# Kernel optimization log

Hardware: AMD Instinct MI355X
Metric: run time of the kernel (lower is better)

Reference implementation:

```python
import jax, jax.numpy as jnp
import numpy as np
from jax import lax

NC = 8  # num_classes
NUM_ITERS = 2


def _resize_bilinear_ac(x, out_h, out_w):
    """Bilinear resize with align_corners=True, x: (N, C, H, W)."""
    N, C, H, W = x.shape

    def coords(n_out, n_in):
        if n_out == 1:
            return jnp.zeros((1,), jnp.float32)
        return jnp.linspace(0.0, float(n_in - 1), n_out, dtype=jnp.float32)

    ys = coords(out_h, H)
    xs = coords(out_w, W)
    y0 = jnp.floor(ys).astype(jnp.int32)
    y1 = jnp.minimum(y0 + 1, H - 1)
    wy = (ys - y0.astype(jnp.float32)).astype(x.dtype)
    x0 = jnp.floor(xs).astype(jnp.int32)
    x1 = jnp.minimum(x0 + 1, W - 1)
    wx = (xs - x0.astype(jnp.float32)).astype(x.dtype)

    r0 = x[:, :, y0, :]
    r1 = x[:, :, y1, :]
    r = r0 * (1.0 - wy)[None, None, :, None] + r1 * wy[None, None, :, None]
    c0 = r[:, :, :, x0]
    c1 = r[:, :, :, x1]
    return c0 * (1.0 - wx)[None, None, None, :] + c1 * wx[None, None, None, :]


def _conv2d(x, w, groups=1):
    k = w.shape[-1]
    pad = k // 2
    return lax.conv_general_dilated(
        x, w, window_strides=(1, 1), padding=[(pad, pad), (pad, pad)],
        dimension_numbers=('NCHW', 'OIHW', 'NCHW'), feature_group_count=groups)


def _mean_field_update(unary, guidance, spatial_w, bilateral_w, compat_w):
    Q = jax.nn.softmax(unary, axis=1)
    cw = compat_w[:, :, 0, 0]  # (O, I)
    for _ in range(NUM_ITERS):
        spatial_msg = _conv2d(Q, spatial_w, groups=NC)          # depthwise 3x3
        bilateral_in = jnp.concatenate([Q, guidance], axis=1)   # (N, NC+6, H, W)
        bilateral_msg = _conv2d(bilateral_in, bilateral_w)      # 3x3 dense
        message = spatial_msg + bilateral_msg
        message = jnp.einsum('nchw,oc->nohw', message, cw)      # 1x1 compat conv
        Q = jax.nn.softmax(unary - message, axis=1)
    return Q


def setup_inputs() -> dict:
    key = jax.random.key(0)
    ks = jax.random.split(key, 16)
    inp = {
        'logits': jax.random.normal(ks[0], (8, NC, 512, 512), jnp.float32),
        'image': jax.random.uniform(ks[1], (8, 3, 512, 512), jnp.float32),
        'skip0': jax.random.normal(ks[2], (8, 64, 256, 256), jnp.float32),
        'skip1': jax.random.normal(ks[3], (8, 128, 128, 128), jnp.float32),
        'skip2': jax.random.normal(ks[4], (8, 256, 64, 64), jnp.float32),
        'skip3': jax.random.normal(ks[5], (8, 512, 32, 32), jnp.float32),
        'spatial_w': jax.random.normal(ks[6], (NC, 1, 3, 3), jnp.float32) * 0.1,
        'bilateral_w': jax.random.normal(ks[7], (NC, NC + 6, 3, 3), jnp.float32) * 0.1,
        # compat_conv is initialized to -I (zeros then -= eye) in the module
        'compat_w': (-jnp.eye(NC, dtype=jnp.float32)).reshape(NC, NC, 1, 1),
        'skip_w0': jax.random.normal(ks[8], (3, 64, 1, 1), jnp.float32) * 0.05,
        'skip_b0': jnp.zeros((3,), jnp.float32),
        'skip_w1': jax.random.normal(ks[9], (3, 128, 1, 1), jnp.float32) * 0.05,
        'skip_b1': jnp.zeros((3,), jnp.float32),
        'skip_w2': jax.random.normal(ks[10], (3, 256, 1, 1), jnp.float32) * 0.05,
        'skip_b2': jnp.zeros((3,), jnp.float32),
        'skip_w3': jax.random.normal(ks[11], (3, 512, 1, 1), jnp.float32) * 0.05,
        'skip_b3': jnp.zeros((3,), jnp.float32),
    }
    return inp


def reference(logits, image, skip0, skip1, skip2, skip3,
              spatial_w, bilateral_w, compat_w,
              skip_w0, skip_b0, skip_w1, skip_b1,
              skip_w2, skip_b2, skip_w3, skip_b3):
    H, W = logits.shape[2], logits.shape[3]

    # fuse_skip_features: 1x1 project each skip to 3ch, upsample, average
    skips = [skip0, skip1, skip2, skip3]
    ws = [skip_w0, skip_w1, skip_w2, skip_w3]
    bs = [skip_b0, skip_b1, skip_b2, skip_b3]
    fused = jnp.zeros((logits.shape[0], 3, H, W), logits.dtype)
    for feat, w, b in zip(skips, ws, bs):
        p = jnp.einsum('nchw,oc->nohw', feat, w[:, :, 0, 0]) + b[None, :, None, None]
        fused = fused + _resize_bilinear_ac(p, H, W)
    fused = fused / len(skips)

    guidance = jnp.concatenate([image, fused], axis=1)  # (N, 6, H, W)

    Q_full = _mean_field_update(logits, guidance, spatial_w, bilateral_w, compat_w)

    logits_down = _resize_bilinear_ac(logits, H // 2, W // 2)
    guidance_down = _resize_bilinear_ac(guidance, H // 2, W // 2)
    Q_down = _mean_field_update(logits_down, guidance_down, spatial_w, bilateral_w, compat_w)
    Q_down_up = _resize_bilinear_ac(Q_down, H, W)

    return (Q_full + Q_down_up) / 2.0
```

## Files before the change

kernel.cpp:

```cpp
#include <hip/hip_runtime.h>
#include <hip/hip_fp16.h>
#include <math.h>

#define NB 8
#define NCLS 8
#define NGU 6
#define NBI 14
#define HF 512
#define WF 512
#define HH 256
#define WH 256

#define TOX 32
#define TOY 16
#define SX 36
#define SY 20
#define SPX (SY * SX)
#define R1W 36
#define R1N (18 * 36)
#define R1T 41
#define R2N (TOX * TOY)
#define R2T 32

typedef _Float16 f16x8 __attribute__((ext_vector_type(8)));
typedef float f32x4 __attribute__((ext_vector_type(4)));

static __device__ __forceinline__ void ac_prep(int o, float scale, int insz,
                                               int& i0, int& i1, float& f) {
    float s = (float)o * scale;
    int ii = (int)floorf(s);
    if (ii > insz - 1) ii = insz - 1;
    if (ii < 0) ii = 0;
    i0 = ii;
    i1 = (ii + 1 < insz) ? (ii + 1) : (insz - 1);
    f = s - (float)ii;
}

__global__ void k_fill_bias(float* __restrict__ out, const float* __restrict__ b, int HW) {
    int total = NB * 3 * HW;
    int idx = blockIdx.x * blockDim.x + threadIdx.x;
    if (idx >= total) return;
    int o = (idx / HW) % 3;
    out[idx] = b[o];
}

template <bool DIRECT>
__global__ void k_skip_proj(const float* __restrict__ feat, const float* __restrict__ w,
                            const float* __restrict__ b, float* __restrict__ out,
                            int C, int HW, int nch) {
    __shared__ float sw[3 * 512];
    for (int i = threadIdx.x; i < 3 * C; i += blockDim.x) sw[i] = w[i];
    __syncthreads();
    int total = NB * HW * nch;
    for (int idx = blockIdx.x * blockDim.x + threadIdx.x; idx < total;
         idx += gridDim.x * blockDim.x) {
        int hw = idx % HW;
        int t = idx / HW;
        int ch = t % nch;
        int n = t / nch;
        int c0 = ch * 64;
        const float* fp = feat + ((size_t)n * C + c0) * HW + hw;
        float a0 = 0.f, a1 = 0.f, a2 = 0.f;
        #pragma unroll 8
        for (int c = 0; c < 64; ++c) {
            float v = fp[(size_t)c * HW];
            a0 = fmaf(sw[c0 + c], v, a0);
            a1 = fmaf(sw[C + c0 + c], v, a1);
            a2 = fmaf(sw[2 * C + c0 + c], v, a2);
        }
        float* op = out + (size_t)n * 3 * HW + hw;
        if (DIRECT) {
            op[0] = b[0] + a0;
            op[HW] = b[1] + a1;
            op[2 * HW] = b[2] + a2;
        } else {
            atomicAdd(&op[0], a0);
            atomicAdd(&op[HW], a1);
            atomicAdd(&op[2 * HW], a2);
        }
    }
}

__global__ void k_fused_guid(const float* __restrict__ image,
                             const float* __restrict__ p0, const float* __restrict__ p1,
                             const float* __restrict__ p2, const float* __restrict__ p3,
                             float* __restrict__ guid) {
    const int HW = HF * WF;
    int total = NB * HW;
    int idx = blockIdx.x * blockDim.x + threadIdx.x;
    if (idx >= total) return;
    int n = idx / HW, r = idx - n * HW;
    int y = r / WF, x = r - y * WF;

    const float* ps[4] = {p0, p1, p2, p3};
    const int ss[4] = {256, 128, 64, 32};
    float f[3] = {0.f, 0.f, 0.f};
    #pragma unroll
    for (int l = 0; l < 4; ++l) {
        int s = ss[l];
        float scale = (float)(s - 1) / 511.0f;
        int y0, y1, x0, x1;
        float fy, fx;
        ac_prep(y, scale, s, y0, y1, fy);
        ac_prep(x, scale, s, x0, x1, fx);
        const float* pb = ps[l] + (size_t)n * 3 * s * s;
        #pragma unroll
        for (int o = 0; o < 3; ++o) {
            const float* pp = pb + (size_t)o * s * s;
            float v00 = pp[y0 * s + x0], v01 = pp[y0 * s + x1];
            float v10 = pp[y1 * s + x0], v11 = pp[y1 * s + x1];
            float r0 = v00 * (1.f - fy) + v10 * fy;
            float r1 = v01 * (1.f - fy) + v11 * fy;
            f[o] += r0 * (1.f - fx) + r1 * fx;
        }
    }
    float* gp = guid + (size_t)n * NGU * HW + y * WF + x;
    const float* ip = image + (size_t)n * 3 * HW + y * WF + x;
    #pragma unroll
    for (int o = 0; o < 3; ++o) gp[(size_t)o * HW] = ip[(size_t)o * HW];
    #pragma unroll
    for (int o = 0; o < 3; ++o) gp[(size_t)(3 + o) * HW] = f[o] * 0.25f;
}

__global__ void k_prep_w(const float* __restrict__ wsp, const float* __restrict__ wbil,
                         const float* __restrict__ cw, float* __restrict__ W2) {
    int i = blockIdx.x * blockDim.x + threadIdx.x;
    if (i >= NBI * 9 * 8) return;
    int o = i & 7;
    int t = (i >> 3) % 9;
    int ci = i / 72;
    float s = 0.f;
    for (int c = 0; c < NCLS; ++c)
        s += cw[o * NCLS + c] * wbil[((size_t)c * NBI + ci) * 9 + t];
    if (ci < NCLS) s += cw[o * NCLS + ci] * wsp[ci * 9 + t];
    W2[ci * 72 + t * 8 + o] = s;
}

__global__ void k_prep_frag(const float* __restrict__ W2, _Float16* __restrict__ wf) {
    int i = blockIdx.x * blockDim.x + threadIdx.x;
    if (i >= 5 * 64) return;
    int j = i >> 6, l = i & 63;
    int col = l & 15, kg = l >> 4;
    #pragma unroll
    for (int e = 0; e < 8; ++e) {
        int k = j * 32 + kg * 8 + e;
        int tap = k >> 4, ci = k & 15;
        float v = (tap < 9 && ci < 14 && col < 8) ? W2[ci * 72 + tap * 8 + col] : 0.f;
        wf[i * 8 + e] = (_Float16)v;
    }
}

template <bool DOWN, bool UPFOLD>
__global__ __launch_bounds__(256, 4) void k_mf_mfma(
    const float* __restrict__ unary, const float* __restrict__ guid,
    const float* __restrict__ Qd, float* __restrict__ Qout,
    const _Float16* __restrict__ wfragG, int H, int W, int Hs, int Ws) {
    __shared__ __align__(16) _Float16 s_t[16 + SPX * 16 + 32];
    __shared__ __align__(16) _Float16 s_msg[R1N * 8];
    _Float16* tb = s_t + 16;

    const int tid = threadIdx.x;
    const int lane = tid & 63;
    const int wv = tid >> 6;
    const int n = blockIdx.z;
    const int gx0 = blockIdx.x * TOX;
    const int gy0 = blockIdx.y * TOY;
    const int HW = H * W;
    const int HWs = Hs * Ws;
    const float* ubase = unary + (size_t)n * NCLS * HWs;
    const float* gbase = guid + (size_t)n * NGU * HWs;

    f16x8 wf[5];
    #pragma unroll
    for (int j = 0; j < 5; ++j)
        wf[j] = *(const f16x8*)(wfragG + (j * 64 + lane) * 8);

    if (tid < 16) s_t[tid] = (_Float16)0.f;
    if (tid >= 16 && tid < 48) s_t[16 + SPX * 16 + (tid - 16)] = (_Float16)0.f;

    const float syc = DOWN ? (float)(Hs - 1) / (float)(H - 1) : 1.f;
    const float sxc = DOWN ? (float)(Ws - 1) / (float)(W - 1) : 1.f;
    for (int i = tid; i < SPX; i += 256) {
        int yy = i / SX, xx = i - yy * SX;
        int gy = gy0 + yy - 2, gx = gx0 + xx - 2;
        f16x8 qv, gv;
        #pragma unroll
        for (int o = 0; o < 8; ++o) { qv[o] = (_Float16)0.f; gv[o] = (_Float16)0.f; }
        if ((unsigned)gy < (unsigned)H && (unsigned)gx < (unsigned)W) {
            float u[8], g[6];
            if (DOWN) {
                int y0, y1, x0, x1;
                float fy, fx;
                ac_prep(gy, syc, Hs, y0, y1, fy);
                ac_prep(gx, sxc, Ws, x0, x1, fx);
                const float w00 = (1.f - fy) * (1.f - fx), w01 = (1.f - fy) * fx;
                const float w10 = fy * (1.f - fx), w11 = fy * fx;
                const size_t o00 = (size_t)y0 * Ws + x0, o01 = (size_t)y0 * Ws + x1;
                const size_t o10 = (size_t)y1 * Ws + x0, o11 = (size_t)y1 * Ws + x1;
                #pragma unroll
                for (int o = 0; o < 8; ++o) {
                    const float* up = ubase + (size_t)o * HWs;
                    u[o] = w00 * up[o00] + w01 * up[o01] + w10 * up[o10] + w11 * up[o11];
                }
                #pragma unroll
                for (int c = 0; c < 6; ++c) {
                    const float* gp = gbase + (size_t)c * HWs;
                    g[c] = w00 * gp[o00] + w01 * gp[o01] + w10 * gp[o10] + w11 * gp[o11];
                }
            } else {
                const size_t off = (size_t)gy * W + gx;
                #pragma unroll
                for (int o = 0; o < 8; ++o) u[o] = ubase[(size_t)o * HWs + off];
                #pragma unroll
                for (int c = 0; c < 6; ++c) g[c] = gbase[(size_t)c * HWs + off];
            }
            float e[8];
            float s = 0.f;
            #pragma unroll
            for (int o = 0; o < 8; ++o) { e[o] = __expf(u[o]); s += e[o]; }
            float inv = 1.f / s;
            #pragma unroll
            for (int o = 0; o < 8; ++o) qv[o] = (_Float16)(e[o] * inv);
            #pragma unroll
            for (int c = 0; c < 6; ++c) gv[c] = (_Float16)g[c];
        }
        *(f16x8*)(tb + i * 16) = qv;
        *(f16x8*)(tb + i * 16 + 8) = gv;
    }
    __syncthreads();

    for (int t = wv; t < R1T; t += 4) {
        int pb = t * 16;
        int p = pb + (lane & 15);
        if (p > R1N - 1) p = R1N - 1;
        int qy = p / R1W;
        int yy = 1 + qy, xx = p - qy * R1W;
        int kg = lane >> 4;
        f32x4 acc = {0.f, 0.f, 0.f, 0.f};
        #pragma unroll
        for (int j = 0; j < 5; ++j) {
            int tap = 2 * j + (kg >> 1);
            if (tap > 8) tap = 8;
            int dy = tap / 3 - 1, dx = tap - (tap / 3) * 3 - 1;
            int idx = (yy + dy) * SX + (xx + dx);
            f16x8 af = *(const f16x8*)(tb + idx * 16 + (kg & 1) * 8);
            acc = __builtin_amdgcn_mfma_f32_16x16x32_f16(af, wf[j], acc, 0, 0, 0);
        }
        int ch = lane & 15;
        if (ch < 8) {
            int pxb = pb + (lane >> 4) * 4;
            #pragma unroll
            for (int r = 0; r < 4; ++r) {
                int px = pxb + r;
                if (px < R1N) s_msg[px * 8 + ch] = (_Float16)acc[r];
            }
        }
    }
    __syncthreads();

    for (int i = tid; i < R1N; i += 256) {
        int qy = i / R1W;
        int yy = 1 + qy, xx = i - qy * R1W;
        int gy = gy0 + yy - 2, gx = gx0 + xx - 2;
        if ((unsigned)gy < (unsigned)H && (unsigned)gx < (unsigned)W) {
            f16x8 m = *(const f16x8*)(s_msg + i * 8);
            f16x8 q0 = *(const f16x8*)(tb + (i + SX) * 16);
            float e[8];
            float s = 0.f;
            #pragma unroll
            for (int o = 0; o < 8; ++o) {
                e[o] = (float)q0[o] * __expf(-(float)m[o]);
                s += e[o];
            }
            float inv = 1.f / s;
            f16x8 q1;
            #pragma unroll
            for (int o = 0; o < 8; ++o) q1[o] = (_Float16)(e[o] * inv);
            *(f16x8*)(tb + (i + SX) * 16) = q1;
        }
    }
    f16x8 m1r[2];
    #pragma unroll
    for (int u2 = 0; u2 < 2; ++u2) {
        int i = tid + 256 * u2;
        int oy = i >> 5, ox = i & 31;
        int r1 = (1 + oy) * R1W + (2 + ox);
        m1r[u2] = *(const f16x8*)(s_msg + r1 * 8);
    }
    __syncthreads();

    for (int t = wv; t < R2T; t += 4) {
        int pb = t * 16;
        int p = pb + (lane & 15);
        int yy = 2 + (p >> 5), xx = 2 + (p & 31);
        int kg = lane >> 4;
        f32x4 acc = {0.f, 0.f, 0.f, 0.f};
        #pragma unroll
        for (int j = 0; j < 5; ++j) {
            int tap = 2 * j + (kg >> 1);
            if (tap > 8) tap = 8;
            int dy = tap / 3 - 1, dx = tap - (tap / 3) * 3 - 1;
            int idx = (yy + dy) * SX + (xx + dx);
            f16x8 af = *(const f16x8*)(tb + idx * 16 + (kg & 1) * 8);
            acc = __builtin_amdgcn_mfma_f32_16x16x32_f16(af, wf[j], acc, 0, 0, 0);
        }
        int ch = lane & 15;
        if (ch < 8) {
            int pxb = pb + (lane >> 4) * 4;
            #pragma unroll
            for (int r = 0; r < 4; ++r) s_msg[(pxb + r) * 8 + ch] = (_Float16)acc[r];
        }
    }
    __syncthreads();

    #pragma unroll
    for (int u2 = 0; u2 < 2; ++u2) {
        int i = tid + 256 * u2;
        int oy = i >> 5, ox = i & 31;
        int gy = gy0 + oy, gx = gx0 + ox;
        f16x8 m2 = *(const f16x8*)(s_msg + i * 8);
        f16x8 q1 = *(const f16x8*)(tb + ((2 + oy) * SX + (2 + ox)) * 16);
        float e[8];
        float s = 0.f;
        #pragma unroll
        for (int o = 0; o < 8; ++o) {
            e[o] = (float)q1[o] * __expf((float)m1r[u2][o] - (float)m2[o]);
            s += e[o];
        }
        float inv = 1.f / s;
        float* qp = Qout + (size_t)n * NCLS * HW + (size_t)gy * W + gx;
        if (UPFOLD) {
            int y0, y1, x0, x1;
            float fy, fx;
            ac_prep(gy, 255.f / 511.f, HH, y0, y1, fy);
            ac_prep(gx, 255.f / 511.f, WH, x0, x1, fx);
            const float w00 = (1.f - fy) * (1.f - fx), w01 = (1.f - fy) * fx;
            const float w10 = fy * (1.f - fx), w11 = fy * fx;
            const size_t o00 = (size_t)y0 * WH + x0, o01 = (size_t)y0 * WH + x1;
            const size_t o10 = (size_t)y1 * WH + x0, o11 = (size_t)y1 * WH + x1;
            const float* qd = Qd + (size_t)n * NCLS * (HH * WH);
            #pragma unroll
            for (int o = 0; o < 8; ++o) {
                const float* qq = qd + (size_t)o * (HH * WH);
                float v = w00 * qq[o00] + w01 * qq[o01] + w10 * qq[o10] + w11 * qq[o11];
                qp[(size_t)o * HW] = fmaf(0.5f, e[o] * inv, 0.5f * v);
            }
        } else {
            #pragma unroll
            for (int o = 0; o < 8; ++o) qp[(size_t)o * HW] = e[o] * inv;
        }
    }
}

static inline int cdiv(int a, int b) { return (a + b - 1) / b; }

extern "C" void kernel_launch(void* const* d_in, const int* in_sizes, int n_in,
                              void* d_out, int out_size, void* d_ws, size_t ws_size,
                              hipStream_t stream) {
    const float* logits = (const float*)d_in[0];
    const float* image = (const float*)d_in[1];
    const float* skip0 = (const float*)d_in[2];
    const float* skip1 = (const float*)d_in[3];
    const float* skip2 = (const float*)d_in[4];
    const float* skip3 = (const float*)d_in[5];
    const float* spatial_w = (const float*)d_in[6];
    const float* bilateral_w = (const float*)d_in[7];
    const float* compat_w = (const float*)d_in[8];
    const float* skip_w0 = (const float*)d_in[9];
    const float* skip_b0 = (const float*)d_in[10];
    const float* skip_w1 = (const float*)d_in[11];
    const float* skip_b1 = (const float*)d_in[12];
    const float* skip_w2 = (const float*)d_in[13];
    const float* skip_b2 = (const float*)d_in[14];
    const float* skip_w3 = (const float*)d_in[15];
    const float* skip_b3 = (const float*)d_in[16];
    float* out = (float*)d_out;
    float* ws = (float*)d_ws;

    float* p0 = ws + 0;
    float* p1 = p0 + (size_t)NB * 3 * 256 * 256;
    float* p2 = p1 + (size_t)NB * 3 * 128 * 128;
    float* p3 = p2 + (size_t)NB * 3 * 64 * 64;
    float* Qa_d = ws + 4194304;
    float* W2 = ws + 16000000;
    _Float16* wfrag = (_Float16*)(ws + 16100000);
    float* guid = ws + 16777216;

    const int HWf = HF * WF;

    k_prep_w<<<4, 256, 0, stream>>>(spatial_w, bilateral_w, compat_w, W2);
    k_prep_frag<<<2, 256, 0, stream>>>(W2, wfrag);

    k_fill_bias<<<cdiv(NB * 3 * 16384, 256), 256, 0, stream>>>(p1, skip_b1, 16384);
    k_fill_bias<<<cdiv(NB * 3 * 4096, 256), 256, 0, stream>>>(p2, skip_b2, 4096);
    k_fill_bias<<<cdiv(NB * 3 * 1024, 256), 256, 0, stream>>>(p3, skip_b3, 1024);

    k_skip_proj<true><<<cdiv(NB * 65536 * 1, 256), 256, 0, stream>>>(skip0, skip_w0, skip_b0, p0, 64, 65536, 1);
    k_skip_proj<false><<<cdiv(NB * 16384 * 2, 256), 256, 0, stream>>>(skip1, skip_w1, skip_b1, p1, 128, 16384, 2);
    k_skip_proj<false><<<cdiv(NB * 4096 * 4, 256), 256, 0, stream>>>(skip2, skip_w2, skip_b2, p2, 256, 4096, 4);
    k_skip_proj<false><<<cdiv(NB * 1024 * 8, 256), 256, 0, stream>>>(skip3, skip_w3, skip_b3, p3, 512, 1024, 8);

    k_fused_guid<<<cdiv(NB * HWf, 256), 256, 0, stream>>>(image, p0, p1, p2, p3, guid);

    {
        dim3 grid(WH / TOX, HH / TOY, NB);
        k_mf_mfma<true, false><<<grid, 256, 0, stream>>>(logits, guid, nullptr, Qa_d,
                                                         wfrag, HH, WH, HF, WF);
    }

    {
        dim3 grid(WF / TOX, HF / TOY, NB);
        k_mf_mfma<false, true><<<grid, 256, 0, stream>>>(logits, guid, Qa_d, out,
                                                         wfrag, HF, WF, HF, WF);
    }
}
```

Before: 235.3 us.

## Store guidance and Q as packed fp16 pixel-interleaved buffers; vectorize skip projection

The guidance tensor and the initial softmax Q are now written once as pixel-interleaved fp16 (8 channels per pixel) by a combined prep kernel, replacing planar fp32 guidance. The mean-field kernels load these with single 16-byte vector loads instead of many strided fp32 loads. The downsampled Q result is also stored as interleaved fp16, which the full-resolution kernel gathers for the upsample fold. The skip projections now process 2 or 4 pixels per thread with vector loads. The aim is to cut global memory traffic and load instruction counts, at the cost of fp16 rounding of guidance and intermediate Q, and an extra full-resolution softmax pass in the prep kernel.

New measurement: 230.6 us. 1.02x faster.

```diff
diff --git a/kernel.cpp b/kernel.cpp
--- a/kernel.cpp
+++ b/kernel.cpp
@@ -19,8 +19,10 @@
 #define R1W 36
 #define R1N (18 * 36)
 #define R1T 41
-#define R2N (TOX * TOY)
 #define R2T 32
+#define PLANE (SPX * 8)
+#define PSTR (PLANE + 32)
+#define TILEH (16 + PSTR + PLANE + 16)
 
 typedef _Float16 f16x8 __attribute__((ext_vector_type(8)));
 typedef float f32x4 __attribute__((ext_vector_type(4)));
@@ -44,51 +46,68 @@
     out[idx] = b[o];
 }
 
-template <bool DIRECT>
+template <int VEC, bool DIRECT>
 __global__ void k_skip_proj(const float* __restrict__ feat, const float* __restrict__ w,
-                            const float* __restrict__ b, float* __restrict__ out,
+                            const float* __restrict__ bias, float* __restrict__ out,
                             int C, int HW, int nch) {
     __shared__ float sw[3 * 512];
     for (int i = threadIdx.x; i < 3 * C; i += blockDim.x) sw[i] = w[i];
     __syncthreads();
-    int total = NB * HW * nch;
+    const int HWv = HW / VEC;
+    int total = NB * HWv * nch;
     for (int idx = blockIdx.x * blockDim.x + threadIdx.x; idx < total;
          idx += gridDim.x * blockDim.x) {
-        int hw = idx % HW;
-        int t = idx / HW;
+        int hv = idx % HWv;
+        int t = idx / HWv;
         int ch = t % nch;
         int n = t / nch;
         int c0 = ch * 64;
-        const float* fp = feat + ((size_t)n * C + c0) * HW + hw;
-        float a0 = 0.f, a1 = 0.f, a2 = 0.f;
-        #pragma unroll 8
+        const float* fp = feat + ((size_t)n * C + c0) * HW + (size_t)hv * VEC;
+        float a[3][VEC];
+        #pragma unroll
+        for (int o = 0; o < 3; ++o)
+            #pragma unroll
+            for (int k = 0; k < VEC; ++k) a[o][k] = 0.f;
+        #pragma unroll 4
         for (int c = 0; c < 64; ++c) {
-            float v = fp[(size_t)c * HW];
-            a0 = fmaf(sw[c0 + c], v, a0);
-            a1 = fmaf(sw[C + c0 + c], v, a1);
-            a2 = fmaf(sw[2 * C + c0 + c], v, a2);
-        }
-        float* op = out + (size_t)n * 3 * HW + hw;
-        if (DIRECT) {
-            op[0] = b[0] + a0;
-            op[HW] = b[1] + a1;
-            op[2 * HW] = b[2] + a2;
-        } else {
-            atomicAdd(&op[0], a0);
-            atomicAdd(&op[HW], a1);
-            atomicAdd(&op[2 * HW], a2);
-        }
-    }
-}
-
-__global__ void k_fused_guid(const float* __restrict__ image,
-                             const float* __restrict__ p0, const float* __restrict__ p1,
-                             const float* __restrict__ p2, const float* __restrict__ p3,
-                             float* __restrict__ guid) {
+            float v[VEC];
+            if constexpr (VEC == 4) {
+                float4 t4 = *reinterpret_cast<const float4*>(fp + (size_t)c * HW);
+                v[0] = t4.x; v[1] = t4.y; v[2] = t4.z; v[3] = t4.w;
+            } else if constexpr (VEC == 2) {
+                float2 t2 = *reinterpret_cast<const float2*>(fp + (size_t)c * HW);
+                v[0] = t2.x; v[1] = t2.y;
+            } else {
+                v[0] = fp[(size_t)c * HW];
+            }
+            #pragma unroll
+            for (int o = 0; o < 3; ++o) {
+                const float wv = sw[o * C + c0 + c];
+                #pragma unroll
+                for (int k = 0; k < VEC; ++k) a[o][k] = fmaf(wv, v[k], a[o][k]);
+            }
+        }
+        float* op = out + (size_t)n * 3 * HW + (size_t)hv * VEC;
+        #pragma unroll
+        for (int o = 0; o < 3; ++o) {
+            #pragma unroll
+            for (int k = 0; k < VEC; ++k) {
+                if (DIRECT)
+                    op[(size_t)o * HW + k] = bias[o] + a[o][k];
+                else
+                    atomicAdd(&op[(size_t)o * HW + k], a[o][k]);
+            }
+        }
+    }
+}
+
+__global__ void k_prep_full(const float* __restrict__ logits, const float* __restrict__ image,
+                            const float* __restrict__ p0, const float* __restrict__ p1,
+                            const float* __restrict__ p2, const float* __restrict__ p3,
+                            _Float16* __restrict__ Gh, _Float16* __restrict__ Q0h) {
     const int HW = HF * WF;
-    int total = NB * HW;
     int idx = blockIdx.x * blockDim.x + threadIdx.x;
-    if (idx >= total) return;
+    if (idx >= NB * HW) return;
     int n = idx / HW, r = idx - n * HW;
     int y = r / WF, x = r - y * WF;
 
@@ -114,12 +133,26 @@
             f[o] += r0 * (1.f - fx) + r1 * fx;
         }
     }
-    float* gp = guid + (size_t)n * NGU * HW + y * WF + x;
-    const float* ip = image + (size_t)n * 3 * HW + y * WF + x;
-    #pragma unroll
-    for (int o = 0; o < 3; ++o) gp[(size_t)o * HW] = ip[(size_t)o * HW];
-    #pragma unroll
-    for (int o = 0; o < 3; ++o) gp[(size_t)(3 + o) * HW] = f[o] * 0.25f;
+    const float* ip = image + (size_t)n * 3 * HW + r;
+    f16x8 gv;
+    #pragma unroll
+    for (int o = 0; o < 3; ++o) gv[o] = (_Float16)ip[(size_t)o * HW];
+    #pragma unroll
+    for (int o = 0; o < 3; ++o) gv[3 + o] = (_Float16)(f[o] * 0.25f);
+    gv[6] = (_Float16)0.f;
+    gv[7] = (_Float16)0.f;
+    *(f16x8*)(Gh + (size_t)idx * 8) = gv;
+
+    const float* up = logits + (size_t)n * NCLS * HW + r;
+    float e[8];
+    float s = 0.f;
+    #pragma unroll
+    for (int o = 0; o < 8; ++o) { e[o] = __expf(up[(size_t)o * HW]); s += e[o]; }
+    float inv = 1.f / s;
+    f16x8 qv;
+    #pragma unroll
+    for (int o = 0; o < 8; ++o) qv[o] = (_Float16)(e[o] * inv);
+    *(f16x8*)(Q0h + (size_t)idx * 8) = qv;
 }
 
 __global__ void k_prep_w(const float* __restrict__ wsp, const float* __restrict__ wbil,
@@ -152,12 +185,14 @@
 
 template <bool DOWN, bool UPFOLD>
 __global__ __launch_bounds__(256, 4) void k_mf_mfma(
-    const float* __restrict__ unary, const float* __restrict__ guid,
-    const float* __restrict__ Qd, float* __restrict__ Qout,
-    const _Float16* __restrict__ wfragG, int H, int W, int Hs, int Ws) {
-    __shared__ __align__(16) _Float16 s_t[16 + SPX * 16 + 32];
+    const float* __restrict__ unary, const _Float16* __restrict__ Q0h,
+    const _Float16* __restrict__ Gh, const _Float16* __restrict__ Qd,
+    void* __restrict__ QoutV, const _Float16* __restrict__ wfragG,
+    int H, int W, int Hs, int Ws) {
+    __shared__ __align__(16) _Float16 s_t[TILEH];
     __shared__ __align__(16) _Float16 s_msg[R1N * 8];
-    _Float16* tb = s_t + 16;
+    _Float16* tb0 = s_t + 16;
+    _Float16* tb1 = s_t + 16 + PSTR;
 
     const int tid = threadIdx.x;
     const int lane = tid & 63;
@@ -167,8 +202,6 @@
     const int gy0 = blockIdx.y * TOY;
     const int HW = H * W;
     const int HWs = Hs * Ws;
-    const float* ubase = unary + (size_t)n * NCLS * HWs;
-    const float* gbase = guid + (size_t)n * NGU * HWs;
 
     f16x8 wf[5];
     #pragma unroll
@@ -176,7 +209,8 @@
         wf[j] = *(const f16x8*)(wfragG + (j * 64 + lane) * 8);
 
     if (tid < 16) s_t[tid] = (_Float16)0.f;
-    if (tid >= 16 && tid < 48) s_t[16 + SPX * 16 + (tid - 16)] = (_Float16)0.f;
+    else if (tid < 48) s_t[5760 + tid] = (_Float16)0.f;
+    else if (tid < 64) s_t[11520 + tid] = (_Float16)0.f;
 
     const float syc = DOWN ? (float)(Hs - 1) / (float)(H - 1) : 1.f;
     const float sxc = DOWN ? (float)(Ws - 1) / (float)(W - 1) : 1.f;
@@ -187,7 +221,6 @@
         #pragma unroll
         for (int o = 0; o < 8; ++o) { qv[o] = (_Float16)0.f; gv[o] = (_Float16)0.f; }
         if ((unsigned)gy < (unsigned)H && (unsigned)gx < (unsigned)W) {
-            float u[8], g[6];
             if (DOWN) {
                 int y0, y1, x0, x1;
                 float fy, fx;
@@ -197,35 +230,38 @@
                 const float w10 = fy * (1.f - fx), w11 = fy * fx;
                 const size_t o00 = (size_t)y0 * Ws + x0, o01 = (size_t)y0 * Ws + x1;
                 const size_t o10 = (size_t)y1 * Ws + x0, o11 = (size_t)y1 * Ws + x1;
+                const float* ubase = unary + (size_t)n * NCLS * HWs;
+                float e[8];
+                float s = 0.f;
                 #pragma unroll
                 for (int o = 0; o < 8; ++o) {
                     const float* up = ubase + (size_t)o * HWs;
-                    u[o] = w00 * up[o00] + w01 * up[o01] + w10 * up[o10] + w11 * up[o11];
+                    float u = w00 * up[o00] + w01 * up[o01] + w10 * up[o10] + w11 * up[o11];
+                    e[o] = __expf(u);
+                    s += e[o];
                 }
+                float inv = 1.f / s;
                 #pragma unroll
-                for (int c = 0; c < 6; ++c) {
-                    const float* gp = gbase + (size_t)c * HWs;
-                    g[c] = w00 * gp[o00] + w01 * gp[o01] + w10 * gp[o10] + w11 * gp[o11];
+                for (int o = 0; o < 8; ++o) qv[o] = (_Float16)(e[o] * inv);
+                const size_t gb = (size_t)n * HWs;
+                f16x8 ga = *(const f16x8*)(Gh + (gb + o00) * 8);
+                f16x8 gb2 = *(const f16x8*)(Gh + (gb + o01) * 8);
+                f16x8 gc = *(const f16x8*)(Gh + (gb + o10) * 8);
+                f16x8 gd = *(const f16x8*)(Gh + (gb + o11) * 8);
+                #pragma unroll
+                for (int c = 0; c < 8; ++c) {
+                    float g = w00 * (float)ga[c] + w01 * (float)gb2[c] +
+                              w10 * (float)gc[c] + w11 * (float)gd[c];
+                    gv[c] = (_Float16)g;
                 }
             } else {
-                const size_t off = (size_t)gy * W + gx;
-                #pragma unroll
-                for (int o = 0; o < 8; ++o) u[o] = ubase[(size_t)o * HWs + off];
-                #pragma unroll
-                for (int c = 0; c < 6; ++c) g[c] = gbase[(size_t)c * HWs + off];
-            }
-            float e[8];
-            float s = 0.f;
-            #pragma unroll
-            for (int o = 0; o < 8; ++o) { e[o] = __expf(u[o]); s += e[o]; }
-            float inv = 1.f / s;
-            #pragma unroll
-            for (int o = 0; o < 8; ++o) qv[o] = (_Float16)(e[o] * inv);
-            #pragma unroll
-            for (int c = 0; c < 6; ++c) gv[c] = (_Float16)g[c];
-        }
-        *(f16x8*)(tb + i * 16) = qv;
-        *(f16x8*)(tb + i * 16 + 8) = gv;
+                const size_t off = ((size_t)n * HW + (size_t)gy * W + gx) * 8;
+                qv = *(const f16x8*)(Q0h + off);
+                gv = *(const f16x8*)(Gh + off);
+            }
+        }
+        *(f16x8*)(tb0 + i * 8) = qv;
+        *(f16x8*)(tb1 + i * 8) = gv;
     }
     __syncthreads();
 
@@ -243,7 +279,7 @@
             if (tap > 8) tap = 8;
             int dy = tap / 3 - 1, dx = tap - (tap / 3) * 3 - 1;
             int idx = (yy + dy) * SX + (xx + dx);
-            f16x8 af = *(const f16x8*)(tb + idx * 16 + (kg & 1) * 8);
+            f16x8 af = *(const f16x8*)(tb0 + (kg & 1) * PSTR + idx * 8);
             acc = __builtin_amdgcn_mfma_f32_16x16x32_f16(af, wf[j], acc, 0, 0, 0);
         }
         int ch = lane & 15;
@@ -264,7 +300,7 @@
         int gy = gy0 + yy - 2, gx = gx0 + xx - 2;
         if ((unsigned)gy < (unsigned)H && (unsigned)gx < (unsigned)W) {
             f16x8 m = *(const f16x8*)(s_msg + i * 8);
-            f16x8 q0 = *(const f16x8*)(tb + (i + SX) * 16);
+            f16x8 q0 = *(const f16x8*)(tb0 + (i + SX) * 8);
             float e[8];
             float s = 0.f;
             #pragma unroll
@@ -276,7 +312,7 @@
             f16x8 q1;
             #pragma unroll
             for (int o = 0; o < 8; ++o) q1[o] = (_Float16)(e[o] * inv);
-            *(f16x8*)(tb + (i + SX) * 16) = q1;
+            *(f16x8*)(tb0 + (i + SX) * 8) = q1;
         }
     }
     f16x8 m1r[2];
@@ -301,7 +337,7 @@
             if (tap > 8) tap = 8;
             int dy = tap / 3 - 1, dx = tap - (tap / 3) * 3 - 1;
             int idx = (yy + dy) * SX + (xx + dx);
-            f16x8 af = *(const f16x8*)(tb + idx * 16 + (kg & 1) * 8);
+            f16x8 af = *(const f16x8*)(tb0 + (kg & 1) * PSTR + idx * 8);
             acc = __builtin_amdgcn_mfma_f32_16x16x32_f16(af, wf[j], acc, 0, 0, 0);
         }
         int ch = lane & 15;
@@ -319,7 +355,7 @@
         int oy = i >> 5, ox = i & 31;
         int gy = gy0 + oy, gx = gx0 + ox;
         f16x8 m2 = *(const f16x8*)(s_msg + i * 8);
-        f16x8 q1 = *(const f16x8*)(tb + ((2 + oy) * SX + (2 + ox)) * 16);
+        f16x8 q1 = *(const f16x8*)(tb0 + ((2 + oy) * SX + (2 + ox)) * 8);
         float e[8];
         float s = 0.f;
         #pragma unroll
@@ -328,26 +364,31 @@
             s += e[o];
         }
         float inv = 1.f / s;
-        float* qp = Qout + (size_t)n * NCLS * HW + (size_t)gy * W + gx;
         if (UPFOLD) {
+            float* qp = (float*)QoutV + (size_t)n * NCLS * HW + (size_t)gy * W + gx;
             int y0, y1, x0, x1;
             float fy, fx;
             ac_prep(gy, 255.f / 511.f, HH, y0, y1, fy);
             ac_prep(gx, 255.f / 511.f, WH, x0, x1, fx);
             const float w00 = (1.f - fy) * (1.f - fx), w01 = (1.f - fy) * fx;
             const float w10 = fy * (1.f - fx), w11 = fy * fx;
-            const size_t o00 = (size_t)y0 * WH + x0, o01 = (size_t)y0 * WH + x1;
-            const size_t o10 = (size_t)y1 * WH + x0, o11 = (size_t)y1 * WH + x1;
-            const float* qd = Qd + (size_t)n * NCLS * (HH * WH);
+            const size_t qb = (size_t)n * (HH * WH);
+            f16x8 qa = *(const f16x8*)(Qd + (qb + (size_t)y0 * WH + x0) * 8);
+            f16x8 qbv = *(const f16x8*)(Qd + (qb + (size_t)y0 * WH + x1) * 8);
+            f16x8 qc = *(const f16x8*)(Qd + (qb + (size_t)y1 * WH + x0) * 8);
+            f16x8 qdv = *(const f16x8*)(Qd + (qb + (size_t)y1 * WH + x1) * 8);
             #pragma unroll
             for (int o = 0; o < 8; ++o) {
-                const float* qq = qd + (size_t)o * (HH * WH);
-                float v = w00 * qq[o00] + w01 * qq[o01] + w10 * qq[o10] + w11 * qq[o11];
+                float v = w00 * (float)qa[o] + w01 * (float)qbv[o] +
+                          w10 * (float)qc[o] + w11 * (float)qdv[o];
                 qp[(size_t)o * HW] = fmaf(0.5f, e[o] * inv, 0.5f * v);
             }
         } else {
-            #pragma unroll
-            for (int o = 0; o < 8; ++o) qp[(size_t)o * HW] = e[o] * inv;
+            _Float16* qo = (_Float16*)QoutV + ((size_t)n * HW + (size_t)gy * W + gx) * 8;
+            f16x8 q2;
+            #pragma unroll
+            for (int o = 0; o < 8; ++o) q2[o] = (_Float16)(e[o] * inv);
+            *(f16x8*)qo = q2;
         }
     }
 }
@@ -378,13 +419,14 @@
     float* ws = (float*)d_ws;
 
     float* p0 = ws + 0;
-    float* p1 = p0 + (size_t)NB * 3 * 256 * 256;
-    float* p2 = p1 + (size_t)NB * 3 * 128 * 128;
-    float* p3 = p2 + (size_t)NB * 3 * 64 * 64;
-    float* Qa_d = ws + 4194304;
-    float* W2 = ws + 16000000;
-    _Float16* wfrag = (_Float16*)(ws + 16100000);
-    float* guid = ws + 16777216;
+    float* p1 = ws + 1572864;
+    float* p2 = ws + 1966080;
+    float* p3 = ws + 2064384;
+    float* W2 = ws + 2100000;
+    _Float16* wfrag = (_Float16*)(ws + 2110000);
+    _Float16* Q0h = (_Float16*)(ws + 4194304);
+    _Float16* Gh = (_Float16*)(ws + 12582912);
+    _Float16* Qdh = (_Float16*)(ws + 20971520);
 
     const int HWf = HF * WF;
 
@@ -395,22 +437,26 @@
     k_fill_bias<<<cdiv(NB * 3 * 4096, 256), 256, 0, stream>>>(p2, skip_b2, 4096);
     k_fill_bias<<<cdiv(NB * 3 * 1024, 256), 256, 0, stream>>>(p3, skip_b3, 1024);
 
-    k_skip_proj<true><<<cdiv(NB * 65536 * 1, 256), 256, 0, stream>>>(skip0, skip_w0, skip_b0, p0, 64, 65536, 1);
-    k_skip_proj<false><<<cdiv(NB * 16384 * 2, 256), 256, 0, stream>>>(skip1, skip_w1, skip_b1, p1, 128, 16384, 2);
-    k_skip_proj<false><<<cdiv(NB * 4096 * 4, 256), 256, 0, stream>>>(skip2, skip_w2, skip_b2, p2, 256, 4096, 4);
-    k_skip_proj<false><<<cdiv(NB * 1024 * 8, 256), 256, 0, stream>>>(skip3, skip_w3, skip_b3, p3, 512, 1024, 8);
-
-    k_fused_guid<<<cdiv(NB * HWf, 256), 256, 0, stream>>>(image, p0, p1, p2, p3, guid);
+    k_skip_proj<4, true><<<cdiv(NB * 16384 * 1, 256), 256, 0, stream>>>(
+        skip0, skip_w0, skip_b0, p0, 64, 65536, 1);
+    k_skip_proj<4, false><<<cdiv(NB * 4096 * 2, 256), 256, 0, stream>>>(
+        skip1, skip_w1, skip_b1, p1, 128, 16384, 2);
+    k_skip_proj<2, false><<<cdiv(NB * 2048 * 4, 256), 256, 0, stream>>>(
+        skip2, skip_w2, skip_b2, p2, 256, 4096, 4);
+    k_skip_proj<1, false><<<cdiv(NB * 1024 * 8, 256), 256, 0, stream>>>(
+        skip3, skip_w3, skip_b3, p3, 512, 1024, 8);
+
+    k_prep_full<<<cdiv(NB * HWf, 256), 256, 0, stream>>>(logits, image, p0, p1, p2, p3, Gh, Q0h);
 
     {
         dim3 grid(WH / TOX, HH / TOY, NB);
-        k_mf_mfma<true, false><<<grid, 256, 0, stream>>>(logits, guid, nullptr, Qa_d,
-                                                         wfrag, HH, WH, HF, WF);
+        k_mf_mfma<true, false><<<grid, 256, 0, stream>>>(
+            logits, nullptr, Gh, nullptr, (void*)Qdh, wfrag, HH, WH, HF, WF);
     }
 
     {
         dim3 grid(WF / TOX, HF / TOY, NB);
-        k_mf_mfma<false, true><<<grid, 256, 0, stream>>>(logits, guid, Qa_d, out,
-                                                         wfrag, HF, WF, HF, WF);
-    }
-}
+        k_mf_mfma<false, true><<<grid, 256, 0, stream>>>(
+            nullptr, Q0h, Gh, Qdh, (void*)out, wfrag, HF, WF, HF, WF);
+    }
+}
```
